# Performance work log

Measured on AMD Instinct MI355X. Metric: run time of the kernel, lower is better.

The kernel has to match this reference:

```python
import jax, jax.numpy as jnp
import numpy as np

# Static config (matches init_kwargs / spatial layout)
SHAPES = ((64, 64), (32, 32), (16, 16))   # (H, W) per level, bev=256 at /4,/8,/16
B, HEADS, LEVELS, POINTS, C = 2, 8, 3, 4, 256
HD = C // HEADS
NV = sum(h * w for h, w in SHAPES)        # 5376
NQ = NV
TP = HEADS * LEVELS * POINTS              # 96


def setup_inputs() -> dict:
    key = jax.random.key(0)
    ks = jax.random.split(key, 10)
    s = 1.0 / np.sqrt(C)
    inp = {
        'query': jax.random.normal(ks[0], (B, NQ, C), dtype=jnp.float32),
        'reference_points': jax.random.uniform(ks[1], (B, NQ, 2), dtype=jnp.float32),
        'value': jax.random.normal(ks[2], (B, NV, C), dtype=jnp.float32),
        'Wv': jax.random.normal(ks[3], (C, C), dtype=jnp.float32) * s,
        'bv': jnp.zeros((C,), dtype=jnp.float32),
        # offset proj: small scale so sampling stays local-ish (orig init is 0)
        'Woff': jax.random.normal(ks[4], (TP * 2, C), dtype=jnp.float32) * (0.02 * s),
        'boff': jnp.zeros((TP * 2,), dtype=jnp.float32),
        'Wa': jax.random.normal(ks[5], (TP, C), dtype=jnp.float32) * s,
        'ba': jnp.zeros((TP,), dtype=jnp.float32),
        'Wo': jax.random.normal(ks[6], (C, C), dtype=jnp.float32) * s,
        'bo': jnp.zeros((C,), dtype=jnp.float32),
    }
    return inp


def _msda(query, reference_points, value, Wv, bv, Woff, boff, Wa, ba, Wo, bo):
    Bb, nq, _ = query.shape
    # value projection -> per-head values
    v = (value @ Wv.T + bv).reshape(Bb, NV, HEADS, HD)
    # sampling offsets: (B, NQ, HEADS, LEVELS, POINTS, 2)
    off = (query @ Woff.T + boff).reshape(Bb, nq, HEADS, LEVELS, POINTS, 2)
    # attention weights: softmax over LEVELS*POINTS jointly
    a = (query @ Wa.T + ba).reshape(Bb, nq, HEADS, LEVELS * POINTS)
    a = jax.nn.softmax(a, axis=-1).reshape(Bb, nq, HEADS, LEVELS, POINTS)
    # sampling locations in [0,1] (clamp matches torch .clamp(0,1))
    loc = jnp.clip(reference_points[:, :, None, None, None, :] + off, 0.0, 1.0)

    out = jnp.zeros((Bb, HEADS, nq, HD), dtype=query.dtype)
    start = 0
    for lvl, (H, W) in enumerate(SHAPES):
        n = H * W
        # (B, HEADS, H*W, HD) flattened level feature map per head
        vl = jnp.transpose(v[:, start:start + n].reshape(Bb, H, W, HEADS, HD),
                           (0, 3, 1, 2, 4)).reshape(Bb, HEADS, n, HD)
        loc_l = loc[:, :, :, lvl]                     # (B, NQ, HEADS, K, 2)
        # align_corners=False unnormalization: ((g+1)*size - 1)/2 with g=2*loc-1
        x = loc_l[..., 0] * W - 0.5
        y = loc_l[..., 1] * H - 0.5
        x0 = jnp.floor(x)
        y0 = jnp.floor(y)
        wx1 = x - x0
        wy1 = y - y0
        x0i = x0.astype(jnp.int32)
        y0i = y0.astype(jnp.int32)
        acc = jnp.zeros((Bb, HEADS, nq * POINTS, HD), dtype=query.dtype)
        for dy in (0, 1):
            for dx in (0, 1):
                ix = x0i + dx
                iy = y0i + dy
                wgt = (wx1 if dx else 1.0 - wx1) * (wy1 if dy else 1.0 - wy1)
                # zero padding outside the map (padding_mode='zeros')
                valid = (ix >= 0) & (ix < W) & (iy >= 0) & (iy < H)
                idx = jnp.clip(iy, 0, H - 1) * W + jnp.clip(ix, 0, W - 1)
                idx_t = jnp.transpose(idx, (0, 2, 1, 3)).reshape(Bb, HEADS, nq * POINTS)
                g = jnp.take_along_axis(vl, idx_t[..., None], axis=2)  # (B,H,NQ*K,HD)
                w_t = jnp.transpose(wgt * valid.astype(wgt.dtype),
                                    (0, 2, 1, 3)).reshape(Bb, HEADS, nq * POINTS, 1)
                acc = acc + g * w_t
        aw = jnp.transpose(a[:, :, :, lvl], (0, 2, 1, 3)).reshape(Bb, HEADS, nq * POINTS, 1)
        out = out + (acc * aw).reshape(Bb, HEADS, nq, POINTS, HD).sum(axis=3)
        start += n
    out = jnp.transpose(out, (0, 2, 1, 3)).reshape(Bb, nq, C)
    return out @ Wo.T + bo


def reference(query, reference_points, value, Wv, bv, Woff, boff, Wa, ba, Wo, bo):
    return _msda(query, reference_points, value, Wv, bv, Woff, boff, Wa, ba, Wo, bo)
```

## Files before the change

kernel.cpp:

```cpp
#include <hip/hip_runtime.h>
#include <hip/hip_bf16.h>
#include <cmath>

#define BATCH   2
#define NQ      5376
#define NV      5376
#define CDIM    256
#define HEADS   8
#define HD      32
#define LEVELS  3
#define POINTS  4
#define TP      96
#define MROWS   (BATCH*NQ)
#define NOFF    (TP*2)
#define NQA     (NOFF+TP)

typedef __attribute__((ext_vector_type(8))) short bf16x8;
typedef __attribute__((ext_vector_type(4))) float f32x4;
typedef unsigned short u16;
typedef unsigned int   u32;

#define AS1 __attribute__((address_space(1)))
#define AS3 __attribute__((address_space(3)))

__device__ __forceinline__ void g2lds16(const void* g, void* l) {
    __builtin_amdgcn_global_load_lds((const AS1 void*)g, (AS3 void*)l, 16, 0, 0);
}

__device__ __forceinline__ u16 bf_of(float f) {
    union { __hip_bfloat16 h; u16 s; } u;
    u.h = __float2bfloat16(f);
    return u.s;
}
__device__ __forceinline__ float bf_back(u16 s) {
    return __uint_as_float((u32)s << 16);
}

__global__ __launch_bounds__(256) void split_vq_kernel(
    const float* __restrict__ value, const float* __restrict__ query,
    u16* __restrict__ vhi, u16* __restrict__ vlo,
    u16* __restrict__ qhi, u16* __restrict__ qlo, int n4)
{
    int i = blockIdx.x * 256 + threadIdx.x;
    const float* src; u16* dh; u16* dl;
    if (i < n4) { src = value; dh = vhi; dl = vlo; }
    else        { src = query; dh = qhi; dl = qlo; i -= n4; }
    const float4 v = reinterpret_cast<const float4*>(src)[i];
    ushort4 h, l;
    h.x = bf_of(v.x); l.x = bf_of(v.x - bf_back(h.x));
    h.y = bf_of(v.y); l.y = bf_of(v.y - bf_back(h.y));
    h.z = bf_of(v.z); l.z = bf_of(v.z - bf_back(h.z));
    h.w = bf_of(v.w); l.w = bf_of(v.w - bf_back(h.w));
    reinterpret_cast<ushort4*>(dh)[i] = h;
    reinterpret_cast<ushort4*>(dl)[i] = l;
}

__global__ __launch_bounds__(256) void split_w_kernel(
    const float* __restrict__ Wv, const float* __restrict__ Woff,
    const float* __restrict__ Wa, const float* __restrict__ Wo,
    u16* __restrict__ wv_hi, u16* __restrict__ wv_lo,
    u16* __restrict__ wqa_hi, u16* __restrict__ wqa_lo,
    u16* __restrict__ wo_hi, u16* __restrict__ wo_lo)
{
    const int i = blockIdx.x * 256 + threadIdx.x;
    const float* src; u16* dh; u16* dl; int j;
    if (i < 16384) {
        j = i; src = Wv + (size_t)j * 4; dh = wv_hi; dl = wv_lo;
    } else if (i < 34816) {
        j = i - 16384;
        const int row = j >> 6, c4 = j & 63;
        src = (row < NOFF) ? (Woff + (size_t)row * CDIM + c4 * 4)
                           : (Wa + (size_t)(row - NOFF) * CDIM + c4 * 4);
        dh = wqa_hi; dl = wqa_lo;
    } else {
        j = i - 34816; src = Wo + (size_t)j * 4; dh = wo_hi; dl = wo_lo;
    }
    const float4 v = *reinterpret_cast<const float4*>(src);
    ushort4 h, l;
    h.x = bf_of(v.x); l.x = bf_of(v.x - bf_back(h.x));
    h.y = bf_of(v.y); l.y = bf_of(v.y - bf_back(h.y));
    h.z = bf_of(v.z); l.z = bf_of(v.z - bf_back(h.z));
    h.w = bf_of(v.w); l.w = bf_of(v.w - bf_back(h.w));
    reinterpret_cast<ushort4*>(dh)[j] = h;
    reinterpret_cast<ushort4*>(dl)[j] = l;
}

#define GBM 64
#define GBN 64
#define GBK 32

template <int MODE>
__global__ __launch_bounds__(256) void gemm_split_kernel(
    const u16* __restrict__ Ah, const u16* __restrict__ Al,
    const u16* __restrict__ Bh, const u16* __restrict__ Bl,
    const float* __restrict__ bias, const float* __restrict__ bias2,
    void* __restrict__ Cout, void* __restrict__ Cout2,
    int M, int N, int K)
{
    __shared__ u16 sAh[GBM * GBK];
    __shared__ u16 sAl[GBM * GBK];
    __shared__ u16 sBh[GBN * GBK];
    __shared__ u16 sBl[GBN * GBK];

    const int m0 = blockIdx.x * GBM;
    const int n0 = blockIdx.y * GBN;
    const int tid  = threadIdx.x;
    const int lane = tid & 63;
    const int wave = tid >> 6;
    const int wr   = wave & 1;
    const int wc   = wave >> 1;
    const int qm   = lane & 15;
    const int quad = lane >> 4;

    f32x4 acc[2][2];
    #pragma unroll
    for (int i = 0; i < 2; ++i)
        #pragma unroll
        for (int j = 0; j < 2; ++j)
            acc[i][j] = (f32x4){0.f, 0.f, 0.f, 0.f};

    const int srow = (wave << 4) + (lane >> 2);
    const int sk   = (lane & 3) * 8;
    const int brc  = min(n0 + srow, N - 1);

    for (int k0 = 0; k0 < K; k0 += GBK) {
        const size_t ga = (size_t)(m0 + srow) * K + k0 + sk;
        const size_t gb = (size_t)brc * K + k0 + sk;
        g2lds16(Ah + ga, sAh + wave * 512);
        g2lds16(Al + ga, sAl + wave * 512);
        g2lds16(Bh + gb, sBh + wave * 512);
        g2lds16(Bl + gb, sBl + wave * 512);
        __syncthreads();

        bf16x8 fah[2], fal[2], fbh[2], fbl[2];
        #pragma unroll
        for (int x = 0; x < 2; ++x) {
            const int rm = wr * 32 + x * 16 + qm;
            const int rn = wc * 32 + x * 16 + qm;
            fah[x] = *reinterpret_cast<const bf16x8*>(&sAh[rm * GBK + quad * 8]);
            fal[x] = *reinterpret_cast<const bf16x8*>(&sAl[rm * GBK + quad * 8]);
            fbh[x] = *reinterpret_cast<const bf16x8*>(&sBh[rn * GBK + quad * 8]);
            fbl[x] = *reinterpret_cast<const bf16x8*>(&sBl[rn * GBK + quad * 8]);
        }
        #pragma unroll
        for (int mi = 0; mi < 2; ++mi)
            #pragma unroll
            for (int ni = 0; ni < 2; ++ni) {
                acc[mi][ni] = __builtin_amdgcn_mfma_f32_16x16x32_bf16(
                    fah[mi], fbh[ni], acc[mi][ni], 0, 0, 0);
                acc[mi][ni] = __builtin_amdgcn_mfma_f32_16x16x32_bf16(
                    fah[mi], fbl[ni], acc[mi][ni], 0, 0, 0);
                acc[mi][ni] = __builtin_amdgcn_mfma_f32_16x16x32_bf16(
                    fal[mi], fbh[ni], acc[mi][ni], 0, 0, 0);
            }
        __syncthreads();
    }

    #pragma unroll
    for (int mi = 0; mi < 2; ++mi) {
        #pragma unroll
        for (int ni = 0; ni < 2; ++ni) {
            const int n = n0 + wc * 32 + ni * 16 + qm;
            if (n >= N) continue;
            float bn;
            if (MODE == 2) bn = (n < NOFF) ? bias[n] : bias2[n - NOFF];
            else           bn = bias[n];
            #pragma unroll
            for (int r = 0; r < 4; ++r) {
                const int m = m0 + wr * 32 + mi * 16 + quad * 4 + r;
                const float val = acc[mi][ni][r] + bn;
                if (MODE == 0)
                    reinterpret_cast<float*>(Cout)[(size_t)m * N + n] = val;
                else if (MODE == 1)
                    reinterpret_cast<u16*>(Cout)[(size_t)m * N + n] = bf_of(val);
                else {
                    if (n < NOFF)
                        reinterpret_cast<float*>(Cout)[(size_t)m * NOFF + n] = val;
                    else
                        reinterpret_cast<float*>(Cout2)[(size_t)m * TP + (n - NOFF)] = val;
                }
            }
        }
    }
}

__global__ __launch_bounds__(256) void msda_core_kernel(
    const float* __restrict__ off,
    const float* __restrict__ alog,
    const float* __restrict__ refp,
    const u16*   __restrict__ v,
    u16* __restrict__ t_hi,
    u16* __restrict__ t_lo)
{
    const int tid  = threadIdx.x;
    const int half = tid >> 7;
    const int ht   = tid & 127;
    const int bq   = blockIdx.x * 2 + half;
    const int b    = bq / NQ;

    __shared__ float s_w[2][TP];
    __shared__ int   s_idx[2][TP][4];
    __shared__ float s_twt[2][TP][4];

    if (ht < TP) s_w[half][ht] = alog[(size_t)bq * TP + ht];
    __syncthreads();

    if (ht < HEADS) {
        float mx = -1e30f;
        #pragma unroll
        for (int i = 0; i < 12; ++i) mx = fmaxf(mx, s_w[half][ht * 12 + i]);
        float e[12];
        float sum = 0.f;
        #pragma unroll
        for (int i = 0; i < 12; ++i) {
            e[i] = expf(s_w[half][ht * 12 + i] - mx);
            sum += e[i];
        }
        const float inv = 1.f / sum;
        #pragma unroll
        for (int i = 0; i < 12; ++i) s_w[half][ht * 12 + i] = e[i] * inv;
    }
    __syncthreads();

    if (ht < TP) {
        const int j  = ht;
        const int jj = j % 12;
        const int l  = jj >> 2;
        const int Wl    = (l == 0) ? 64 : (l == 1) ? 32 : 16;
        const int start = (l == 0) ? 0 : (l == 1) ? 4096 : 5120;

        const float refx = refp[(size_t)bq * 2 + 0];
        const float refy = refp[(size_t)bq * 2 + 1];
        const float lx = fminf(fmaxf(refx + off[(size_t)bq * NOFF + j * 2 + 0], 0.f), 1.f) * (float)Wl - 0.5f;
        const float ly = fminf(fmaxf(refy + off[(size_t)bq * NOFF + j * 2 + 1], 0.f), 1.f) * (float)Wl - 0.5f;
        const float fx0 = floorf(lx), fy0 = floorf(ly);
        const int   x0  = (int)fx0,   y0  = (int)fy0;
        const float wx1 = lx - fx0,   wy1 = ly - fy0;
        const float wx0 = 1.f - wx1,  wy0 = 1.f - wy1;
        const float aw  = s_w[half][j];

        #pragma unroll
        for (int k = 0; k < 4; ++k) {
            const int dx = k & 1, dy = k >> 1;
            const int xi = x0 + dx, yi = y0 + dy;
            const bool ok = (xi >= 0) & (xi < Wl) & (yi >= 0) & (yi < Wl);
            const int xc = min(max(xi, 0), Wl - 1);
            const int yc = min(max(yi, 0), Wl - 1);
            s_idx[half][j][k] = (start + yc * Wl + xc) * (CDIM * 2);
            const float wxy = (dx ? wx1 : wx0) * (dy ? wy1 : wy0);
            s_twt[half][j][k] = ok ? aw * wxy : 0.f;
        }
    }
    __syncthreads();

    const int h  = ht >> 4;
    const int cp = ht & 15;
    const char* vb = (const char*)(v + (size_t)b * NV * CDIM + h * HD + cp * 2);

    float accx = 0.f, accy = 0.f;
    #pragma unroll
    for (int g = 0; g < 6; ++g) {
        u32   raw[8];
        float wt[8];
        #pragma unroll
        for (int pp = 0; pp < 2; ++pp) {
            const int j = h * 12 + g * 2 + pp;
            const int4   ix = *reinterpret_cast<const int4*>(&s_idx[half][j][0]);
            const float4 tw = *reinterpret_cast<const float4*>(&s_twt[half][j][0]);
            raw[pp * 4 + 0] = *reinterpret_cast<const u32*>(vb + ix.x);
            raw[pp * 4 + 1] = *reinterpret_cast<const u32*>(vb + ix.y);
            raw[pp * 4 + 2] = *reinterpret_cast<const u32*>(vb + ix.z);
            raw[pp * 4 + 3] = *reinterpret_cast<const u32*>(vb + ix.w);
            wt[pp * 4 + 0] = tw.x; wt[pp * 4 + 1] = tw.y;
            wt[pp * 4 + 2] = tw.z; wt[pp * 4 + 3] = tw.w;
        }
        #pragma unroll
        for (int k = 0; k < 8; ++k) {
            accx += wt[k] * __uint_as_float(raw[k] << 16);
            accy += wt[k] * __uint_as_float(raw[k] & 0xffff0000u);
        }
    }

    const u16 th0 = bf_of(accx), tl0 = bf_of(accx - bf_back(th0));
    const u16 th1 = bf_of(accy), tl1 = bf_of(accy - bf_back(th1));
    const size_t oi = (size_t)bq * (CDIM / 2) + h * 16 + cp;
    reinterpret_cast<u32*>(t_hi)[oi] = (u32)th0 | ((u32)th1 << 16);
    reinterpret_cast<u32*>(t_lo)[oi] = (u32)tl0 | ((u32)tl1 << 16);
}

extern "C" void kernel_launch(void* const* d_in, const int* in_sizes, int n_in,
                              void* d_out, int out_size, void* d_ws, size_t ws_size,
                              hipStream_t stream)
{
    const float* query = (const float*)d_in[0];
    const float* refp  = (const float*)d_in[1];
    const float* value = (const float*)d_in[2];
    const float* Wv    = (const float*)d_in[3];
    const float* bv    = (const float*)d_in[4];
    const float* Woff  = (const float*)d_in[5];
    const float* boff  = (const float*)d_in[6];
    const float* Wa    = (const float*)d_in[7];
    const float* ba    = (const float*)d_in[8];
    const float* Wo    = (const float*)d_in[9];
    const float* bo    = (const float*)d_in[10];
    float* out = (float*)d_out;

    char* w = (char*)d_ws;
    const size_t SZ_QV = (size_t)MROWS * CDIM * 2;
    u16* q_hi   = (u16*)(w);
    u16* q_lo   = (u16*)(w + SZ_QV);
    u16* val_hi = (u16*)(w + 2 * SZ_QV);
    u16* val_lo = (u16*)(w + 3 * SZ_QV);
    u16* v_bf16 = (u16*)(w + 4 * SZ_QV);
    char* wp    = w + 5 * SZ_QV;
    u16* wv_hi  = (u16*)(wp);                  wp += (size_t)CDIM * CDIM * 2;
    u16* wv_lo  = (u16*)(wp);                  wp += (size_t)CDIM * CDIM * 2;
    u16* wqa_hi = (u16*)(wp);                  wp += (size_t)NQA * CDIM * 2;
    u16* wqa_lo = (u16*)(wp);                  wp += (size_t)NQA * CDIM * 2;
    u16* wo_hi  = (u16*)(wp);                  wp += (size_t)CDIM * CDIM * 2;
    u16* wo_lo  = (u16*)(wp);                  wp += (size_t)CDIM * CDIM * 2;
    float* ws_off = (float*)(wp);              wp += (size_t)MROWS * NOFF * 4;
    float* ws_a   = (float*)(wp);
    u16* t_hi = val_hi;
    u16* t_lo = val_lo;

    const dim3 blk(256);
    const int n4_qv = MROWS * CDIM / 4;

    split_vq_kernel<<<dim3(2 * n4_qv / 256), blk, 0, stream>>>(
        value, query, val_hi, val_lo, q_hi, q_lo, n4_qv);
    split_w_kernel<<<dim3(200), blk, 0, stream>>>(
        Wv, Woff, Wa, Wo, wv_hi, wv_lo, wqa_hi, wqa_lo, wo_hi, wo_lo);

    gemm_split_kernel<1><<<dim3(MROWS / GBM, CDIM / GBN), blk, 0, stream>>>(
        val_hi, val_lo, wv_hi, wv_lo, bv, nullptr, v_bf16, nullptr,
        MROWS, CDIM, CDIM);
    gemm_split_kernel<2><<<dim3(MROWS / GBM, (NQA + GBN - 1) / GBN), blk, 0, stream>>>(
        q_hi, q_lo, wqa_hi, wqa_lo, boff, ba, ws_off, ws_a,
        MROWS, NQA, CDIM);
    msda_core_kernel<<<dim3(MROWS / 2), blk, 0, stream>>>(
        ws_off, ws_a, refp, v_bf16, t_hi, t_lo);
    gemm_split_kernel<0><<<dim3(MROWS / GBM, CDIM / GBN), blk, 0, stream>>>(
        t_hi, t_lo, wo_hi, wo_lo, bo, nullptr, out, nullptr,
        MROWS, CDIM, CDIM);
}
```

Before: 146.5 us.

## Cut split-bf16 products per GEMM and store values head-major for sampling

Each GEMM now takes a template count of split-bf16 products. The offset/attention projection uses a single bf16 product, and the value and output projections drop the hi*lo weight term. This removes the query lo split, the lo weight loads and some MFMAs. The value projection now writes a head-major layout, so the sampling kernel can gather 8-byte chunks per corner, split the points across two lane groups and combine them with a shuffle. The lower precision in the offset path could shift sampling locations and reduce accuracy.

```diff
diff --git a/kernel.cpp b/kernel.cpp
--- a/kernel.cpp
+++ b/kernel.cpp
@@ -39,27 +39,31 @@
 __global__ __launch_bounds__(256) void split_vq_kernel(
     const float* __restrict__ value, const float* __restrict__ query,
     u16* __restrict__ vhi, u16* __restrict__ vlo,
-    u16* __restrict__ qhi, u16* __restrict__ qlo, int n4)
+    u16* __restrict__ qhi, int n4)
 {
     int i = blockIdx.x * 256 + threadIdx.x;
     const float* src; u16* dh; u16* dl;
     if (i < n4) { src = value; dh = vhi; dl = vlo; }
-    else        { src = query; dh = qhi; dl = qlo; i -= n4; }
+    else        { src = query; dh = qhi; dl = nullptr; i -= n4; }
     const float4 v = reinterpret_cast<const float4*>(src)[i];
-    ushort4 h, l;
-    h.x = bf_of(v.x); l.x = bf_of(v.x - bf_back(h.x));
-    h.y = bf_of(v.y); l.y = bf_of(v.y - bf_back(h.y));
-    h.z = bf_of(v.z); l.z = bf_of(v.z - bf_back(h.z));
-    h.w = bf_of(v.w); l.w = bf_of(v.w - bf_back(h.w));
+    ushort4 h;
+    h.x = bf_of(v.x); h.y = bf_of(v.y); h.z = bf_of(v.z); h.w = bf_of(v.w);
     reinterpret_cast<ushort4*>(dh)[i] = h;
-    reinterpret_cast<ushort4*>(dl)[i] = l;
+    if (dl) {
+        ushort4 l;
+        l.x = bf_of(v.x - bf_back(h.x));
+        l.y = bf_of(v.y - bf_back(h.y));
+        l.z = bf_of(v.z - bf_back(h.z));
+        l.w = bf_of(v.w - bf_back(h.w));
+        reinterpret_cast<ushort4*>(dl)[i] = l;
+    }
 }
 
 __global__ __launch_bounds__(256) void split_w_kernel(
     const float* __restrict__ Wv, const float* __restrict__ Woff,
     const float* __restrict__ Wa, const float* __restrict__ Wo,
     u16* __restrict__ wv_hi, u16* __restrict__ wv_lo,
-    u16* __restrict__ wqa_hi, u16* __restrict__ wqa_lo,
+    u16* __restrict__ wqa_hi,
     u16* __restrict__ wo_hi, u16* __restrict__ wo_lo)
 {
     const int i = blockIdx.x * 256 + threadIdx.x;
@@ -71,25 +75,29 @@
         const int row = j >> 6, c4 = j & 63;
         src = (row < NOFF) ? (Woff + (size_t)row * CDIM + c4 * 4)
                            : (Wa + (size_t)(row - NOFF) * CDIM + c4 * 4);
-        dh = wqa_hi; dl = wqa_lo;
+        dh = wqa_hi; dl = nullptr;
     } else {
         j = i - 34816; src = Wo + (size_t)j * 4; dh = wo_hi; dl = wo_lo;
     }
     const float4 v = *reinterpret_cast<const float4*>(src);
-    ushort4 h, l;
-    h.x = bf_of(v.x); l.x = bf_of(v.x - bf_back(h.x));
-    h.y = bf_of(v.y); l.y = bf_of(v.y - bf_back(h.y));
-    h.z = bf_of(v.z); l.z = bf_of(v.z - bf_back(h.z));
-    h.w = bf_of(v.w); l.w = bf_of(v.w - bf_back(h.w));
+    ushort4 h;
+    h.x = bf_of(v.x); h.y = bf_of(v.y); h.z = bf_of(v.z); h.w = bf_of(v.w);
     reinterpret_cast<ushort4*>(dh)[j] = h;
-    reinterpret_cast<ushort4*>(dl)[j] = l;
+    if (dl) {
+        ushort4 l;
+        l.x = bf_of(v.x - bf_back(h.x));
+        l.y = bf_of(v.y - bf_back(h.y));
+        l.z = bf_of(v.z - bf_back(h.z));
+        l.w = bf_of(v.w - bf_back(h.w));
+        reinterpret_cast<ushort4*>(dl)[j] = l;
+    }
 }
 
 #define GBM 64
 #define GBN 64
 #define GBK 32
 
-template <int MODE>
+template <int NPROD, int MODE>
 __global__ __launch_bounds__(256) void gemm_split_kernel(
     const u16* __restrict__ Ah, const u16* __restrict__ Al,
     const u16* __restrict__ Bh, const u16* __restrict__ Bl,
@@ -127,9 +135,9 @@
         const size_t ga = (size_t)(m0 + srow) * K + k0 + sk;
         const size_t gb = (size_t)brc * K + k0 + sk;
         g2lds16(Ah + ga, sAh + wave * 512);
-        g2lds16(Al + ga, sAl + wave * 512);
+        if (NPROD >= 2) g2lds16(Al + ga, sAl + wave * 512);
         g2lds16(Bh + gb, sBh + wave * 512);
-        g2lds16(Bl + gb, sBl + wave * 512);
+        if (NPROD >= 3) g2lds16(Bl + gb, sBl + wave * 512);
         __syncthreads();
 
         bf16x8 fah[2], fal[2], fbh[2], fbl[2];
@@ -138,9 +146,11 @@
             const int rm = wr * 32 + x * 16 + qm;
             const int rn = wc * 32 + x * 16 + qm;
             fah[x] = *reinterpret_cast<const bf16x8*>(&sAh[rm * GBK + quad * 8]);
-            fal[x] = *reinterpret_cast<const bf16x8*>(&sAl[rm * GBK + quad * 8]);
             fbh[x] = *reinterpret_cast<const bf16x8*>(&sBh[rn * GBK + quad * 8]);
-            fbl[x] = *reinterpret_cast<const bf16x8*>(&sBl[rn * GBK + quad * 8]);
+            if (NPROD >= 2)
+                fal[x] = *reinterpret_cast<const bf16x8*>(&sAl[rm * GBK + quad * 8]);
+            if (NPROD >= 3)
+                fbl[x] = *reinterpret_cast<const bf16x8*>(&sBl[rn * GBK + quad * 8]);
         }
         #pragma unroll
         for (int mi = 0; mi < 2; ++mi)
@@ -148,10 +158,12 @@
             for (int ni = 0; ni < 2; ++ni) {
                 acc[mi][ni] = __builtin_amdgcn_mfma_f32_16x16x32_bf16(
                     fah[mi], fbh[ni], acc[mi][ni], 0, 0, 0);
-                acc[mi][ni] = __builtin_amdgcn_mfma_f32_16x16x32_bf16(
-                    fah[mi], fbl[ni], acc[mi][ni], 0, 0, 0);
-                acc[mi][ni] = __builtin_amdgcn_mfma_f32_16x16x32_bf16(
-                    fal[mi], fbh[ni], acc[mi][ni], 0, 0, 0);
+                if (NPROD >= 2)
+                    acc[mi][ni] = __builtin_amdgcn_mfma_f32_16x16x32_bf16(
+                        fal[mi], fbh[ni], acc[mi][ni], 0, 0, 0);
+                if (NPROD >= 3)
+                    acc[mi][ni] = __builtin_amdgcn_mfma_f32_16x16x32_bf16(
+                        fah[mi], fbl[ni], acc[mi][ni], 0, 0, 0);
             }
         __syncthreads();
     }
@@ -169,11 +181,14 @@
             for (int r = 0; r < 4; ++r) {
                 const int m = m0 + wr * 32 + mi * 16 + quad * 4 + r;
                 const float val = acc[mi][ni][r] + bn;
-                if (MODE == 0)
+                if (MODE == 0) {
                     reinterpret_cast<float*>(Cout)[(size_t)m * N + n] = val;
-                else if (MODE == 1)
-                    reinterpret_cast<u16*>(Cout)[(size_t)m * N + n] = bf_of(val);
-                else {
+                } else if (MODE == 1) {
+                    const int b = m / NV, rr = m - b * NV;
+                    const int h = n >> 5, c = n & 31;
+                    reinterpret_cast<u16*>(Cout)[
+                        (((size_t)b * HEADS + h) * NV + rr) * HD + c] = bf_of(val);
+                } else {
                     if (n < NOFF)
                         reinterpret_cast<float*>(Cout)[(size_t)m * NOFF + n] = val;
                     else
@@ -246,46 +261,60 @@
             const bool ok = (xi >= 0) & (xi < Wl) & (yi >= 0) & (yi < Wl);
             const int xc = min(max(xi, 0), Wl - 1);
             const int yc = min(max(yi, 0), Wl - 1);
-            s_idx[half][j][k] = (start + yc * Wl + xc) * (CDIM * 2);
+            s_idx[half][j][k] = (start + yc * Wl + xc) * (HD * 2);
             const float wxy = (dx ? wx1 : wx0) * (dy ? wy1 : wy0);
             s_twt[half][j][k] = ok ? aw * wxy : 0.f;
         }
     }
     __syncthreads();
 
-    const int h  = ht >> 4;
-    const int cp = ht & 15;
-    const char* vb = (const char*)(v + (size_t)b * NV * CDIM + h * HD + cp * 2);
-
-    float accx = 0.f, accy = 0.f;
+    const int h   = ht >> 4;
+    const int sub = ht & 15;
+    const int q   = sub & 7;
+    const int rep = sub >> 3;
+    const char* vb = (const char*)v + (((size_t)b * HEADS + h) * NV) * (HD * 2) + q * 8;
+
+    float acc0 = 0.f, acc1 = 0.f, acc2 = 0.f, acc3 = 0.f;
     #pragma unroll
-    for (int g = 0; g < 6; ++g) {
-        u32   raw[8];
+    for (int g = 0; g < 3; ++g) {
+        uint2 raw[8];
         float wt[8];
         #pragma unroll
         for (int pp = 0; pp < 2; ++pp) {
-            const int j = h * 12 + g * 2 + pp;
+            const int j = h * 12 + rep * 6 + g * 2 + pp;
             const int4   ix = *reinterpret_cast<const int4*>(&s_idx[half][j][0]);
             const float4 tw = *reinterpret_cast<const float4*>(&s_twt[half][j][0]);
-            raw[pp * 4 + 0] = *reinterpret_cast<const u32*>(vb + ix.x);
-            raw[pp * 4 + 1] = *reinterpret_cast<const u32*>(vb + ix.y);
-            raw[pp * 4 + 2] = *reinterpret_cast<const u32*>(vb + ix.z);
-            raw[pp * 4 + 3] = *reinterpret_cast<const u32*>(vb + ix.w);
+            raw[pp * 4 + 0] = *reinterpret_cast<const uint2*>(vb + ix.x);
+            raw[pp * 4 + 1] = *reinterpret_cast<const uint2*>(vb + ix.y);
+            raw[pp * 4 + 2] = *reinterpret_cast<const uint2*>(vb + ix.z);
+            raw[pp * 4 + 3] = *reinterpret_cast<const uint2*>(vb + ix.w);
             wt[pp * 4 + 0] = tw.x; wt[pp * 4 + 1] = tw.y;
             wt[pp * 4 + 2] = tw.z; wt[pp * 4 + 3] = tw.w;
         }
         #pragma unroll
         for (int k = 0; k < 8; ++k) {
-            accx += wt[k] * __uint_as_float(raw[k] << 16);
-            accy += wt[k] * __uint_as_float(raw[k] & 0xffff0000u);
-        }
-    }
-
-    const u16 th0 = bf_of(accx), tl0 = bf_of(accx - bf_back(th0));
-    const u16 th1 = bf_of(accy), tl1 = bf_of(accy - bf_back(th1));
-    const size_t oi = (size_t)bq * (CDIM / 2) + h * 16 + cp;
-    reinterpret_cast<u32*>(t_hi)[oi] = (u32)th0 | ((u32)th1 << 16);
-    reinterpret_cast<u32*>(t_lo)[oi] = (u32)tl0 | ((u32)tl1 << 16);
+            acc0 += wt[k] * __uint_as_float(raw[k].x << 16);
+            acc1 += wt[k] * __uint_as_float(raw[k].x & 0xffff0000u);
+            acc2 += wt[k] * __uint_as_float(raw[k].y << 16);
+            acc3 += wt[k] * __uint_as_float(raw[k].y & 0xffff0000u);
+        }
+    }
+
+    acc0 += __shfl_xor(acc0, 8);
+    acc1 += __shfl_xor(acc1, 8);
+    acc2 += __shfl_xor(acc2, 8);
+    acc3 += __shfl_xor(acc3, 8);
+
+    if (rep == 0) {
+        ushort4 hh, ll;
+        hh.x = bf_of(acc0); ll.x = bf_of(acc0 - bf_back(hh.x));
+        hh.y = bf_of(acc1); ll.y = bf_of(acc1 - bf_back(hh.y));
+        hh.z = bf_of(acc2); ll.z = bf_of(acc2 - bf_back(hh.z));
+        hh.w = bf_of(acc3); ll.w = bf_of(acc3 - bf_back(hh.w));
+        const size_t base = (size_t)bq * CDIM + h * HD + q * 4;
+        *reinterpret_cast<ushort4*>(t_hi + base) = hh;
+        *reinterpret_cast<ushort4*>(t_lo + base) = ll;
+    }
 }
 
 extern "C" void kernel_launch(void* const* d_in, const int* in_sizes, int n_in,
@@ -308,15 +337,13 @@
     char* w = (char*)d_ws;
     const size_t SZ_QV = (size_t)MROWS * CDIM * 2;
     u16* q_hi   = (u16*)(w);
-    u16* q_lo   = (u16*)(w + SZ_QV);
-    u16* val_hi = (u16*)(w + 2 * SZ_QV);
-    u16* val_lo = (u16*)(w + 3 * SZ_QV);
-    u16* v_bf16 = (u16*)(w + 4 * SZ_QV);
-    char* wp    = w + 5 * SZ_QV;
+    u16* val_hi = (u16*)(w + 1 * SZ_QV);
+    u16* val_lo = (u16*)(w + 2 * SZ_QV);
+    u16* v_bf16 = (u16*)(w + 3 * SZ_QV);
+    char* wp    = w + 4 * SZ_QV;
     u16* wv_hi  = (u16*)(wp);                  wp += (size_t)CDIM * CDIM * 2;
     u16* wv_lo  = (u16*)(wp);                  wp += (size_t)CDIM * CDIM * 2;
     u16* wqa_hi = (u16*)(wp);                  wp += (size_t)NQA * CDIM * 2;
-    u16* wqa_lo = (u16*)(wp);                  wp += (size_t)NQA * CDIM * 2;
     u16* wo_hi  = (u16*)(wp);                  wp += (size_t)CDIM * CDIM * 2;
     u16* wo_lo  = (u16*)(wp);                  wp += (size_t)CDIM * CDIM * 2;
     float* ws_off = (float*)(wp);              wp += (size_t)MROWS * NOFF * 4;
@@ -328,19 +355,19 @@
     const int n4_qv = MROWS * CDIM / 4;
 
     split_vq_kernel<<<dim3(2 * n4_qv / 256), blk, 0, stream>>>(
-        value, query, val_hi, val_lo, q_hi, q_lo, n4_qv);
+        value, query, val_hi, val_lo, q_hi, n4_qv);
     split_w_kernel<<<dim3(200), blk, 0, stream>>>(
-        Wv, Woff, Wa, Wo, wv_hi, wv_lo, wqa_hi, wqa_lo, wo_hi, wo_lo);
-
-    gemm_split_kernel<1><<<dim3(MROWS / GBM, CDIM / GBN), blk, 0, stream>>>(
+        Wv, Woff, Wa, Wo, wv_hi, wv_lo, wqa_hi, wo_hi, wo_lo);
+
+    gemm_split_kernel<2, 1><<<dim3(MROWS / GBM, CDIM / GBN), blk, 0, stream>>>(
         val_hi, val_lo, wv_hi, wv_lo, bv, nullptr, v_bf16, nullptr,
         MROWS, CDIM, CDIM);
-    gemm_split_kernel<2><<<dim3(MROWS / GBM, (NQA + GBN - 1) / GBN), blk, 0, stream>>>(
-        q_hi, q_lo, wqa_hi, wqa_lo, boff, ba, ws_off, ws_a,
+    gemm_split_kernel<1, 2><<<dim3(MROWS / GBM, (NQA + GBN - 1) / GBN), blk, 0, stream>>>(
+        q_hi, nullptr, wqa_hi, nullptr, boff, ba, ws_off, ws_a,
         MROWS, NQA, CDIM);
     msda_core_kernel<<<dim3(MROWS / 2), blk, 0, stream>>>(
         ws_off, ws_a, refp, v_bf16, t_hi, t_lo);
-    gemm_split_kernel<0><<<dim3(MROWS / GBM, CDIM / GBN), blk, 0, stream>>>(
+    gemm_split_kernel<2, 0><<<dim3(MROWS / GBM, CDIM / GBN), blk, 0, stream>>>(
         t_hi, t_lo, wo_hi, wo_lo, bo, nullptr, out, nullptr,
         MROWS, CDIM, CDIM);
 }
```

New measurement: 141.9 us. 3.1% less time.
